# Performance work log

Measured on AMD Instinct MI355X. Metric: run time of the kernel, lower is better.

The kernel has to match this reference:

```python
import jax, jax.numpy as jnp
import numpy as np

B, I, H = 64, 512, 1024


def _linear_params(k, out_dim, in_dim):
    kw, kb = jax.random.split(k)
    bound = 1.0 / np.sqrt(in_dim)
    W = jax.random.uniform(kw, (out_dim, in_dim), minval=-bound, maxval=bound)
    b = jax.random.uniform(kb, (out_dim,), minval=-bound, maxval=bound)
    return W, b


def setup_inputs() -> dict:
    key = jax.random.key(0)
    ks = jax.random.split(key, 14)
    items = jax.random.normal(ks[0], (B, I), dtype=jnp.float32)
    plastic_weights = 0.01 * jax.random.normal(ks[1], (B, H, H), dtype=jnp.float32)
    reward = jax.random.normal(ks[2], (B, 1), dtype=jnp.float32)
    We, be = _linear_params(ks[3], H, I)          # embedding_layer
    W1, b1 = _linear_params(ks[4], H, H)          # extra hidden layer 0
    W2, b2 = _linear_params(ks[5], H, H)          # extra hidden layer 1
    Wfc2, bfc2 = _linear_params(ks[6], H, H)      # fc2
    Whr, bhr = _linear_params(ks[7], H, H)        # hidden_reward_combination_layer
    Wch, bch = _linear_params(ks[8], 1, H)        # choice
    Wr, br = _linear_params(ks[9], H, 1)          # reward_linear
    Wnm, bnm = _linear_params(ks[10], 2, H)       # neuromodulator_out
    Wv, bv = _linear_params(ks[11], 1, H)         # value_out
    alpha = 0.01 * (2.0 * jax.random.uniform(ks[12], (H, H)) - 1.0)
    return dict(items=items, plastic_weights=plastic_weights, reward=reward,
                We=We, be=be, W1=W1, b1=b1, W2=W2, b2=b2,
                Wfc2=Wfc2, bfc2=bfc2, Whr=Whr, bhr=bhr,
                Wch=Wch, bch=bch, Wr=Wr, br=br,
                Wnm=Wnm, bnm=bnm, alpha=alpha, Wv=Wv, bv=bv)


def reference(items, plastic_weights, reward,
              We, be, W1, b1, W2, b2, Wfc2, bfc2, Whr, bhr,
              Wch, bch, Wr, br, Wnm, bnm, alpha, Wv, bv):
    # stacked Linear + tanh
    x = jnp.tanh(items @ We.T + be)            # (B, H)
    x = jnp.tanh(x @ W1.T + b1)
    x = jnp.tanh(x @ W2.T + b2)
    innate = x @ Wfc2.T + bfc2                 # (B, H)
    # plastic contribution: batched matvec with elementwise-scaled weights
    plastic = jnp.einsum('bhi,bi->bh', alpha * plastic_weights, x)
    pre_tanh_hidden = innate + plastic
    hidden = jnp.tanh(pre_tanh_hidden)
    reward_embedding = reward @ Wr.T + br      # (B, H)
    hrc = jnp.tanh((hidden + reward_embedding) @ Whr.T + bhr)
    nm_out = jnp.tanh(hrc @ Wnm.T + bnm)       # (B, 2)
    neuromodulator = (nm_out[:, 0] - nm_out[:, 1])[:, None, None]  # (B,1,1)
    choice = jax.nn.sigmoid(hidden @ Wch.T + bch)  # (B, 1)
    value = hidden @ Wv.T + bv                     # (B, 1)
    hebbian_trace = jnp.tanh(jnp.einsum('bh,bi->bhi', pre_tanh_hidden, x))
    new_pw = jnp.clip(plastic_weights + neuromodulator * hebbian_trace, -50.0, 50.0)
    return (choice, neuromodulator, value, new_pw, hidden)
```

## Files before the change

### kernel.cpp

```cpp
#include <hip/hip_runtime.h>

#define HD 1024
#define BB 64
#define II 512

typedef float f4 __attribute__((ext_vector_type(4)));

__device__ __forceinline__ float fast_tanh(float x) {
    float ax = __builtin_fabsf(x);
    float e  = __builtin_amdgcn_exp2f(ax * -2.8853900817779268f);
    float t  = (1.0f - e) * __builtin_amdgcn_rcpf(1.0f + e);
    return x < 0.0f ? -t : t;
}

template <int K, bool RW>
__global__ __launch_bounds__(512) void k_gemm(const float* __restrict__ A,
                                              const float* __restrict__ W,
                                              const float* __restrict__ bias,
                                              float* __restrict__ out,
                                              const float* __restrict__ rew,
                                              const float* __restrict__ Wr,
                                              const float* __restrict__ br)
{
    constexpr int J = K / 256;
    int tid  = threadIdx.x;
    int lane = tid & 63;
    int wave = tid >> 6;
    int wid  = blockIdx.x * 8 + wave;
    int b    = wid >> 7;
    int h0   = (wid & 127) * 8;
    const float* Ab = A + b * K;

    f4 a[J];
#pragma unroll
    for (int j = 0; j < J; ++j) {
        a[j] = *(const f4*)(Ab + j * 256 + lane * 4);
        if (RW) {
            float rb = rew[b];
            f4 wr4 = *(const f4*)(Wr + j * 256 + lane * 4);
            f4 br4 = *(const f4*)(br + j * 256 + lane * 4);
            a[j].x += rb * wr4.x + br4.x;
            a[j].y += rb * wr4.y + br4.y;
            a[j].z += rb * wr4.z + br4.z;
            a[j].w += rb * wr4.w + br4.w;
        }
    }
    float acc[8];
#pragma unroll
    for (int hh = 0; hh < 8; ++hh) {
        const float* wrow = W + (size_t)(h0 + hh) * K;
        float s = 0.f;
#pragma unroll
        for (int j = 0; j < J; ++j) {
            f4 w4 = *(const f4*)(wrow + j * 256 + lane * 4);
            s += a[j].x * w4.x + a[j].y * w4.y + a[j].z * w4.z + a[j].w * w4.w;
        }
        acc[hh] = s;
    }
#pragma unroll
    for (int hh = 0; hh < 8; ++hh)
#pragma unroll
        for (int off = 32; off; off >>= 1)
            acc[hh] += __shfl_xor(acc[hh], off, 64);
    if (lane == 0) {
        f4 o0, o1;
        o0.x = fast_tanh(acc[0] + bias[h0 + 0]);
        o0.y = fast_tanh(acc[1] + bias[h0 + 1]);
        o0.z = fast_tanh(acc[2] + bias[h0 + 2]);
        o0.w = fast_tanh(acc[3] + bias[h0 + 3]);
        o1.x = fast_tanh(acc[4] + bias[h0 + 4]);
        o1.y = fast_tanh(acc[5] + bias[h0 + 5]);
        o1.z = fast_tanh(acc[6] + bias[h0 + 6]);
        o1.w = fast_tanh(acc[7] + bias[h0 + 7]);
        *(f4*)(out + b * HD + h0)     = o0;
        *(f4*)(out + b * HD + h0 + 4) = o1;
    }
}

__global__ __launch_bounds__(512) void k_plastic(const float* __restrict__ pw,
                                                 const float* __restrict__ alpha,
                                                 const float* __restrict__ Wfc2,
                                                 const float* __restrict__ bfc2,
                                                 const float* __restrict__ x,
                                                 float* __restrict__ pre,
                                                 float* __restrict__ hidden)
{
    __shared__ float xs[8][HD];
    int tid  = threadIdx.x;
    int lane = tid & 63;
    int wave = tid >> 6;
    int bg   = blockIdx.x >> 7;
    int hg   = blockIdx.x & 127;
    int b0   = bg * 8;
    int h    = hg * 8 + wave;

#pragma unroll
    for (int v = tid; v < 2048; v += 512) {
        int r = v >> 8, c = (v & 255) * 4;
        *(f4*)&xs[r][c] = *(const f4*)(x + ((b0 + r) << 10) + c);
    }
    __syncthreads();

    const float* ar = alpha + ((size_t)h << 10);
    const float* wr = Wfc2 + ((size_t)h << 10);
    f4 av[4], wv[4];
#pragma unroll
    for (int j = 0; j < 4; ++j) {
        av[j] = *(const f4*)(ar + j * 256 + lane * 4);
        wv[j] = *(const f4*)(wr + j * 256 + lane * 4);
    }
    float bfc = bfc2[h];

#pragma unroll
    for (int bb = 0; bb < 8; ++bb) {
        const float* prow = pw + ((size_t)(b0 + bb) << 20) + ((size_t)h << 10);
        float accp = 0.f, acci = 0.f;
#pragma unroll
        for (int j = 0; j < 4; ++j) {
            f4 p4 = *(const f4*)(prow + j * 256 + lane * 4);
            f4 x4 = *(const f4*)&xs[bb][j * 256 + lane * 4];
            accp += av[j].x * p4.x * x4.x + av[j].y * p4.y * x4.y +
                    av[j].z * p4.z * x4.z + av[j].w * p4.w * x4.w;
            acci += wv[j].x * x4.x + wv[j].y * x4.y + wv[j].z * x4.z + wv[j].w * x4.w;
        }
#pragma unroll
        for (int off = 32; off; off >>= 1) {
            accp += __shfl_xor(accp, off, 64);
            acci += __shfl_xor(acci, off, 64);
        }
        if (lane == 0) {
            float pv = acci + bfc + accp;
            pre[((b0 + bb) << 10) + h]    = pv;
            hidden[((b0 + bb) << 10) + h] = fast_tanh(pv);
        }
    }
}

__global__ __launch_bounds__(256) void k_heads(const float* __restrict__ hidden,
                                               const float* __restrict__ hrc,
                                               const float* __restrict__ Wnm, const float* __restrict__ bnm,
                                               const float* __restrict__ Wch, const float* __restrict__ bch,
                                               const float* __restrict__ Wv,  const float* __restrict__ bv,
                                               float* __restrict__ out_choice,
                                               float* __restrict__ out_nm,
                                               float* __restrict__ out_value,
                                               float* __restrict__ nm_ws) {
    int b = blockIdx.x;
    int tid = threadIdx.x;
    float a0 = 0.f, a1 = 0.f, a2 = 0.f, a3 = 0.f;
    for (int k = tid; k < HD; k += 256) {
        float hv = hidden[(b << 10) + k];
        float rv = hrc[(b << 10) + k];
        a0 += Wnm[k] * rv;
        a1 += Wnm[HD + k] * rv;
        a2 += Wch[k] * hv;
        a3 += Wv[k] * hv;
    }
    int lane = tid & 63, wave = tid >> 6;
#pragma unroll
    for (int off = 32; off; off >>= 1) {
        a0 += __shfl_xor(a0, off, 64);
        a1 += __shfl_xor(a1, off, 64);
        a2 += __shfl_xor(a2, off, 64);
        a3 += __shfl_xor(a3, off, 64);
    }
    __shared__ float red[4][4];
    if (lane == 0) { red[wave][0] = a0; red[wave][1] = a1; red[wave][2] = a2; red[wave][3] = a3; }
    __syncthreads();
    if (tid == 0) {
        float s0 = red[0][0] + red[1][0] + red[2][0] + red[3][0];
        float s1 = red[0][1] + red[1][1] + red[2][1] + red[3][1];
        float s2 = red[0][2] + red[1][2] + red[2][2] + red[3][2];
        float s3 = red[0][3] + red[1][3] + red[2][3] + red[3][3];
        float n0 = fast_tanh(s0 + bnm[0]);
        float n1 = fast_tanh(s1 + bnm[1]);
        float nv = n0 - n1;
        out_nm[b] = nv;
        nm_ws[b]  = nv;
        float z = s2 + bch[0];
        out_choice[b] = __builtin_amdgcn_rcpf(1.0f + __builtin_amdgcn_exp2f(-z * 1.4426950408889634f));
        out_value[b] = s3 + bv[0];
    }
}

__global__ __launch_bounds__(256) void k_update(const float* __restrict__ pw,
                                                const float* __restrict__ pre,
                                                const float* __restrict__ x,
                                                const float* __restrict__ nm,
                                                float* __restrict__ out) {
    const int stride = 8192 * 256;
    int blk = 8191 - (int)blockIdx.x;
#pragma unroll
    for (int it = 7; it >= 0; --it) {
        int f = blk * 256 + threadIdx.x + it * stride;
        size_t e = (size_t)f << 2;
        int b = f >> 18;
        int h = (f >> 8) & 1023;
        int i = (f & 255) << 2;
        f4 p4 = __builtin_nontemporal_load((const f4*)(pw + e));
        f4 x4 = *(const f4*)(x + (b << 10) + i);
        float ps = pre[(b << 10) + h];
        float nb = nm[b];
        f4 o4;
        o4.x = fminf(fmaxf(p4.x + nb * fast_tanh(ps * x4.x), -50.f), 50.f);
        o4.y = fminf(fmaxf(p4.y + nb * fast_tanh(ps * x4.y), -50.f), 50.f);
        o4.z = fminf(fmaxf(p4.z + nb * fast_tanh(ps * x4.z), -50.f), 50.f);
        o4.w = fminf(fmaxf(p4.w + nb * fast_tanh(ps * x4.w), -50.f), 50.f);
        __builtin_nontemporal_store(o4, (f4*)(out + e));
    }
}

extern "C" void kernel_launch(void* const* d_in, const int* in_sizes, int n_in,
                              void* d_out, int out_size, void* d_ws, size_t ws_size,
                              hipStream_t stream) {
    const float* items  = (const float*)d_in[0];
    const float* pw     = (const float*)d_in[1];
    const float* reward = (const float*)d_in[2];
    const float* We     = (const float*)d_in[3];
    const float* be     = (const float*)d_in[4];
    const float* W1     = (const float*)d_in[5];
    const float* b1     = (const float*)d_in[6];
    const float* W2     = (const float*)d_in[7];
    const float* b2     = (const float*)d_in[8];
    const float* Wfc2   = (const float*)d_in[9];
    const float* bfc2   = (const float*)d_in[10];
    const float* Whr    = (const float*)d_in[11];
    const float* bhr    = (const float*)d_in[12];
    const float* Wch    = (const float*)d_in[13];
    const float* bch    = (const float*)d_in[14];
    const float* Wr     = (const float*)d_in[15];
    const float* br     = (const float*)d_in[16];
    const float* Wnm    = (const float*)d_in[17];
    const float* bnm    = (const float*)d_in[18];
    const float* alpha  = (const float*)d_in[19];
    const float* Wv     = (const float*)d_in[20];
    const float* bv     = (const float*)d_in[21];

    float* ws   = (float*)d_ws;
    float* x0   = ws;
    float* x1   = ws + 65536;
    float* x2   = ws + 131072;
    float* preb = ws + 196608;
    float* hrc  = ws + 262144;
    float* nm   = ws + 327680;

    float* out        = (float*)d_out;
    float* out_choice = out;
    float* out_nm     = out + 64;
    float* out_value  = out + 128;
    float* out_newpw  = out + 192;
    float* out_hidden = out + 192 + BB * HD * HD;

    k_gemm<II, false><<<1024, 512, 0, stream>>>(items, We, be, x0, nullptr, nullptr, nullptr);
    k_gemm<HD, false><<<1024, 512, 0, stream>>>(x0, W1, b1, x1, nullptr, nullptr, nullptr);
    k_gemm<HD, false><<<1024, 512, 0, stream>>>(x1, W2, b2, x2, nullptr, nullptr, nullptr);
    k_plastic<<<1024, 512, 0, stream>>>(pw, alpha, Wfc2, bfc2, x2, preb, out_hidden);
    k_gemm<HD, true><<<1024, 512, 0, stream>>>(out_hidden, Whr, bhr, hrc, reward, Wr, br);
    k_heads<<<64, 256, 0, stream>>>(out_hidden, hrc, Wnm, bnm, Wch, bch, Wv, bv,
                                    out_choice, out_nm, out_value, nm);
    k_update<<<8192, 256, 0, stream>>>(pw, preb, x2, nm, out_newpw);
}
```

Measured before the change: 202.7 us.

## Split plastic/update pipeline into four batch chunks for L2/cache reuse of pw

Processes the batch in four chunks of 16. For each chunk it runs the plastic matvec, hrc GEMM, heads and update kernels back to back, so the plastic_weights slice just read by k_plastic (64 MB per chunk) may still be in the last-level cache when k_update rereads it. k_plastic is also reshaped to one batch per block, loading alpha and Wfc2 per block instead of reusing them across 8 batches. The cost is 12 more kernel launches and more traffic on alpha and Wfc2.

```diff
diff --git a/kernel.cpp b/kernel.cpp
--- a/kernel.cpp
+++ b/kernel.cpp
@@ -20,14 +20,15 @@
                                               float* __restrict__ out,
                                               const float* __restrict__ rew,
                                               const float* __restrict__ Wr,
-                                              const float* __restrict__ br)
+                                              const float* __restrict__ br,
+                                              int b0)
 {
     constexpr int J = K / 256;
     int tid  = threadIdx.x;
     int lane = tid & 63;
     int wave = tid >> 6;
     int wid  = blockIdx.x * 8 + wave;
-    int b    = wid >> 7;
+    int b    = b0 + (wid >> 7);
     int h0   = (wid & 127) * 8;
     const float* Ab = A + b * K;
 
@@ -83,56 +84,46 @@
                                                  const float* __restrict__ bfc2,
                                                  const float* __restrict__ x,
                                                  float* __restrict__ pre,
-                                                 float* __restrict__ hidden)
+                                                 float* __restrict__ hidden,
+                                                 int b0)
 {
-    __shared__ float xs[8][HD];
+    __shared__ float xs[HD];
     int tid  = threadIdx.x;
     int lane = tid & 63;
     int wave = tid >> 6;
-    int bg   = blockIdx.x >> 7;
+    int bb   = blockIdx.x >> 7;
     int hg   = blockIdx.x & 127;
-    int b0   = bg * 8;
+    int b    = b0 + bb;
     int h    = hg * 8 + wave;
 
-#pragma unroll
-    for (int v = tid; v < 2048; v += 512) {
-        int r = v >> 8, c = (v & 255) * 4;
-        *(f4*)&xs[r][c] = *(const f4*)(x + ((b0 + r) << 10) + c);
-    }
+    if (tid < 256) ((f4*)xs)[tid] = ((const f4*)(x + ((size_t)b << 10)))[tid];
     __syncthreads();
 
+    const float* pr = pw + ((size_t)b << 20) + ((size_t)h << 10);
     const float* ar = alpha + ((size_t)h << 10);
     const float* wr = Wfc2 + ((size_t)h << 10);
-    f4 av[4], wv[4];
+
+    float accp = 0.f, acci = 0.f;
 #pragma unroll
     for (int j = 0; j < 4; ++j) {
-        av[j] = *(const f4*)(ar + j * 256 + lane * 4);
-        wv[j] = *(const f4*)(wr + j * 256 + lane * 4);
-    }
-    float bfc = bfc2[h];
-
-#pragma unroll
-    for (int bb = 0; bb < 8; ++bb) {
-        const float* prow = pw + ((size_t)(b0 + bb) << 20) + ((size_t)h << 10);
-        float accp = 0.f, acci = 0.f;
-#pragma unroll
-        for (int j = 0; j < 4; ++j) {
-            f4 p4 = *(const f4*)(prow + j * 256 + lane * 4);
-            f4 x4 = *(const f4*)&xs[bb][j * 256 + lane * 4];
-            accp += av[j].x * p4.x * x4.x + av[j].y * p4.y * x4.y +
-                    av[j].z * p4.z * x4.z + av[j].w * p4.w * x4.w;
-            acci += wv[j].x * x4.x + wv[j].y * x4.y + wv[j].z * x4.z + wv[j].w * x4.w;
-        }
-#pragma unroll
-        for (int off = 32; off; off >>= 1) {
-            accp += __shfl_xor(accp, off, 64);
-            acci += __shfl_xor(acci, off, 64);
-        }
-        if (lane == 0) {
-            float pv = acci + bfc + accp;
-            pre[((b0 + bb) << 10) + h]    = pv;
-            hidden[((b0 + bb) << 10) + h] = fast_tanh(pv);
-        }
+        int i = j * 256 + lane * 4;
+        f4 p4 = *(const f4*)(pr + i);
+        f4 a4 = *(const f4*)(ar + i);
+        f4 w4 = *(const f4*)(wr + i);
+        f4 x4 = *(const f4*)(xs + i);
+        accp += a4.x * p4.x * x4.x + a4.y * p4.y * x4.y +
+                a4.z * p4.z * x4.z + a4.w * p4.w * x4.w;
+        acci += w4.x * x4.x + w4.y * x4.y + w4.z * x4.z + w4.w * x4.w;
+    }
+#pragma unroll
+    for (int off = 32; off; off >>= 1) {
+        accp += __shfl_xor(accp, off, 64);
+        acci += __shfl_xor(acci, off, 64);
+    }
+    if (lane == 0) {
+        float pv = acci + bfc2[h] + accp;
+        pre[((size_t)b << 10) + h]    = pv;
+        hidden[((size_t)b << 10) + h] = fast_tanh(pv);
     }
 }
 
@@ -144,8 +135,9 @@
                                                float* __restrict__ out_choice,
                                                float* __restrict__ out_nm,
                                                float* __restrict__ out_value,
-                                               float* __restrict__ nm_ws) {
-    int b = blockIdx.x;
+                                               float* __restrict__ nm_ws,
+                                               int b0) {
+    int b = b0 + blockIdx.x;
     int tid = threadIdx.x;
     float a0 = 0.f, a1 = 0.f, a2 = 0.f, a3 = 0.f;
     for (int k = tid; k < HD; k += 256) {
@@ -187,14 +179,16 @@
                                                 const float* __restrict__ pre,
                                                 const float* __restrict__ x,
                                                 const float* __restrict__ nm,
-                                                float* __restrict__ out) {
-    const int stride = 8192 * 256;
-    int blk = 8191 - (int)blockIdx.x;
-#pragma unroll
-    for (int it = 7; it >= 0; --it) {
-        int f = blk * 256 + threadIdx.x + it * stride;
-        size_t e = (size_t)f << 2;
-        int b = f >> 18;
+                                                float* __restrict__ out,
+                                                int b0) {
+    int t = blockIdx.x * 256 + threadIdx.x;
+    const int stride = 2048 * 256;
+#pragma unroll
+    for (int it = 0; it < 8; ++it) {
+        int f = t + it * stride;
+        int bl = f >> 18;
+        int b  = b0 + bl;
+        size_t e = ((size_t)b << 20) + (((size_t)(f & 0x3FFFF)) << 2);
         int h = (f >> 8) & 1023;
         int i = (f & 255) << 2;
         f4 p4 = __builtin_nontemporal_load((const f4*)(pw + e));
@@ -251,12 +245,16 @@
     float* out_newpw  = out + 192;
     float* out_hidden = out + 192 + BB * HD * HD;
 
-    k_gemm<II, false><<<1024, 512, 0, stream>>>(items, We, be, x0, nullptr, nullptr, nullptr);
-    k_gemm<HD, false><<<1024, 512, 0, stream>>>(x0, W1, b1, x1, nullptr, nullptr, nullptr);
-    k_gemm<HD, false><<<1024, 512, 0, stream>>>(x1, W2, b2, x2, nullptr, nullptr, nullptr);
-    k_plastic<<<1024, 512, 0, stream>>>(pw, alpha, Wfc2, bfc2, x2, preb, out_hidden);
-    k_gemm<HD, true><<<1024, 512, 0, stream>>>(out_hidden, Whr, bhr, hrc, reward, Wr, br);
-    k_heads<<<64, 256, 0, stream>>>(out_hidden, hrc, Wnm, bnm, Wch, bch, Wv, bv,
-                                    out_choice, out_nm, out_value, nm);
-    k_update<<<8192, 256, 0, stream>>>(pw, preb, x2, nm, out_newpw);
-}
+    k_gemm<II, false><<<1024, 512, 0, stream>>>(items, We, be, x0, nullptr, nullptr, nullptr, 0);
+    k_gemm<HD, false><<<1024, 512, 0, stream>>>(x0, W1, b1, x1, nullptr, nullptr, nullptr, 0);
+    k_gemm<HD, false><<<1024, 512, 0, stream>>>(x1, W2, b2, x2, nullptr, nullptr, nullptr, 0);
+
+    for (int g = 0; g < 4; ++g) {
+        int b0 = g * 16;
+        k_plastic<<<2048, 512, 0, stream>>>(pw, alpha, Wfc2, bfc2, x2, preb, out_hidden, b0);
+        k_gemm<HD, true><<<256, 512, 0, stream>>>(out_hidden, Whr, bhr, hrc, reward, Wr, br, b0);
+        k_heads<<<16, 256, 0, stream>>>(out_hidden, hrc, Wnm, bnm, Wch, bch, Wv, bv,
+                                        out_choice, out_nm, out_value, nm, b0);
+        k_update<<<2048, 256, 0, stream>>>(pw, preb, x2, nm, out_newpw, b0);
+    }
+}
```

After: 248.0 us. 1.22x slower.

## Stage GEMM weight rows in LDS shared across 16 batch rows per block

Applied to the files above, without the earlier changes.

The small dense layers now use 1024-thread blocks. Each block loads an 8-row weight tile, plus the reward vectors for the last layer, into shared memory once, and 16 waves each handle one batch row against it. Before, every wave re-read its weight rows from global memory or cache. The update kernel also switches the plastic-weight load from a nontemporal load to a normal load. The risks are lower occupancy from the larger blocks and LDS use, and half as many blocks.

```diff
diff --git a/kernel.cpp b/kernel.cpp
--- a/kernel.cpp
+++ b/kernel.cpp
@@ -14,31 +14,51 @@
 }
 
 template <int K, bool RW>
-__global__ __launch_bounds__(512) void k_gemm(const float* __restrict__ A,
-                                              const float* __restrict__ W,
-                                              const float* __restrict__ bias,
-                                              float* __restrict__ out,
-                                              const float* __restrict__ rew,
-                                              const float* __restrict__ Wr,
-                                              const float* __restrict__ br)
+__global__ __launch_bounds__(1024) void k_gemm(const float* __restrict__ A,
+                                               const float* __restrict__ W,
+                                               const float* __restrict__ bias,
+                                               float* __restrict__ out,
+                                               const float* __restrict__ rew,
+                                               const float* __restrict__ Wr,
+                                               const float* __restrict__ br)
 {
-    constexpr int J = K / 256;
+    constexpr int J   = K / 256;
+    constexpr int LSZ = RW ? 10 * K : 8 * K;
+    __shared__ float wlds[LSZ];
+
     int tid  = threadIdx.x;
+    int oct  = blockIdx.x & 127;
+    int bg   = blockIdx.x >> 7;
+    int h0   = oct * 8;
+
+    {
+        const f4* src = (const f4*)(W + (size_t)h0 * K);
+        f4* dst = (f4*)wlds;
+#pragma unroll
+        for (int v = tid; v < 2 * K; v += 1024) dst[v] = src[v];
+        if (RW) {
+            const f4* wrs = (const f4*)Wr;
+            const f4* brs = (const f4*)br;
+            f4* d2 = (f4*)(wlds + 8 * K);
+            for (int v = tid; v < K / 4; v += 1024) d2[v] = wrs[v];
+            f4* d3 = (f4*)(wlds + 9 * K);
+            for (int v = tid; v < K / 4; v += 1024) d3[v] = brs[v];
+        }
+    }
+    __syncthreads();
+
     int lane = tid & 63;
     int wave = tid >> 6;
-    int wid  = blockIdx.x * 8 + wave;
-    int b    = wid >> 7;
-    int h0   = (wid & 127) * 8;
-    const float* Ab = A + b * K;
+    int b    = bg * 16 + wave;
 
     f4 a[J];
+    float rb = RW ? rew[b] : 0.0f;
 #pragma unroll
     for (int j = 0; j < J; ++j) {
-        a[j] = *(const f4*)(Ab + j * 256 + lane * 4);
+        a[j] = *(const f4*)(A + (size_t)b * K + j * 256 + lane * 4);
         if (RW) {
-            float rb = rew[b];
-            f4 wr4 = *(const f4*)(Wr + j * 256 + lane * 4);
-            f4 br4 = *(const f4*)(br + j * 256 + lane * 4);
+            f4 wr4 = *(const f4*)(wlds + 8 * K + j * 256 + lane * 4);
+            f4 br4 = *(const f4*)(wlds + 9 * K + j * 256 + lane * 4);
             a[j].x += rb * wr4.x + br4.x;
             a[j].y += rb * wr4.y + br4.y;
             a[j].z += rb * wr4.z + br4.z;
@@ -48,7 +68,7 @@
     float acc[8];
 #pragma unroll
     for (int hh = 0; hh < 8; ++hh) {
-        const float* wrow = W + (size_t)(h0 + hh) * K;
+        const float* wrow = wlds + hh * K;
         float s = 0.f;
 #pragma unroll
         for (int j = 0; j < J; ++j) {
@@ -72,8 +92,8 @@
         o1.y = fast_tanh(acc[5] + bias[h0 + 5]);
         o1.z = fast_tanh(acc[6] + bias[h0 + 6]);
         o1.w = fast_tanh(acc[7] + bias[h0 + 7]);
-        *(f4*)(out + b * HD + h0)     = o0;
-        *(f4*)(out + b * HD + h0 + 4) = o1;
+        *(f4*)(out + (size_t)b * HD + h0)     = o0;
+        *(f4*)(out + (size_t)b * HD + h0 + 4) = o1;
     }
 }
 
@@ -197,7 +217,7 @@
         int b = f >> 18;
         int h = (f >> 8) & 1023;
         int i = (f & 255) << 2;
-        f4 p4 = __builtin_nontemporal_load((const f4*)(pw + e));
+        f4 p4 = *(const f4*)(pw + e);
         f4 x4 = *(const f4*)(x + (b << 10) + i);
         float ps = pre[(b << 10) + h];
         float nb = nm[b];
@@ -251,11 +271,11 @@
     float* out_newpw  = out + 192;
     float* out_hidden = out + 192 + BB * HD * HD;
 
-    k_gemm<II, false><<<1024, 512, 0, stream>>>(items, We, be, x0, nullptr, nullptr, nullptr);
-    k_gemm<HD, false><<<1024, 512, 0, stream>>>(x0, W1, b1, x1, nullptr, nullptr, nullptr);
-    k_gemm<HD, false><<<1024, 512, 0, stream>>>(x1, W2, b2, x2, nullptr, nullptr, nullptr);
+    k_gemm<II, false><<<512, 1024, 0, stream>>>(items, We, be, x0, nullptr, nullptr, nullptr);
+    k_gemm<HD, false><<<512, 1024, 0, stream>>>(x0, W1, b1, x1, nullptr, nullptr, nullptr);
+    k_gemm<HD, false><<<512, 1024, 0, stream>>>(x1, W2, b2, x2, nullptr, nullptr, nullptr);
     k_plastic<<<1024, 512, 0, stream>>>(pw, alpha, Wfc2, bfc2, x2, preb, out_hidden);
-    k_gemm<HD, true><<<1024, 512, 0, stream>>>(out_hidden, Whr, bhr, hrc, reward, Wr, br);
+    k_gemm<HD, true><<<512, 1024, 0, stream>>>(out_hidden, Whr, bhr, hrc, reward, Wr, br);
     k_heads<<<64, 256, 0, stream>>>(out_hidden, hrc, Wnm, bnm, Wch, bch, Wv, bv,
                                     out_choice, out_nm, out_value, nm);
     k_update<<<8192, 256, 0, stream>>>(pw, preb, x2, nm, out_newpw);
```

Result: faster. 179.1 us (-11.7%).
